# Performance work log

Hardware: AMD Instinct MI355X
Metric: run time of the kernel (lower is better)

Reference implementation:

```python
import jax, jax.numpy as jnp
from jax import lax
import numpy as np

S = 2048      # seq_len
E = 1024      # embedding_dim
H = 512       # hidden per direction (hidden_dim // 2)
V = 50000     # vocab
T = 16        # tagset_size
START, STOP = 0, 1
NEG = -10000.0


def setup_inputs() -> dict:
    key = jax.random.key(0)
    ks = jax.random.split(key, 20)
    bound = 1.0 / np.sqrt(H)

    def u(k, shape):
        return jax.random.uniform(k, shape, minval=-bound, maxval=bound, dtype=jnp.float32)

    sentence = jax.random.randint(ks[0], (S,), 0, V)
    emb = jax.random.normal(ks[1], (V, E), dtype=jnp.float32) * 0.1
    # PyTorch LSTM weights, gate order (i, f, g, o) stacked along first dim
    Wih_f = u(ks[2], (4 * H, E)); Whh_f = u(ks[3], (4 * H, H))
    bih_f = u(ks[4], (4 * H,));   bhh_f = u(ks[5], (4 * H,))
    Wih_b = u(ks[6], (4 * H, E)); Whh_b = u(ks[7], (4 * H, H))
    bih_b = u(ks[8], (4 * H,));   bhh_b = u(ks[9], (4 * H,))
    # init_hidden(): randn initial (h0, c0), [2 directions, H] (batch=1 squeezed)
    h0 = jax.random.normal(ks[10], (2, H), dtype=jnp.float32)
    c0 = jax.random.normal(ks[11], (2, H), dtype=jnp.float32)
    Wout = u(ks[12], (T, 2 * H)); bout = u(ks[13], (T,))
    transitions = jax.random.normal(ks[14], (T, T), dtype=jnp.float32)
    transitions = transitions.at[START, :].set(NEG).at[:, STOP].set(NEG)
    return dict(sentence=sentence, emb=emb,
                Wih_f=Wih_f, Whh_f=Whh_f, bih_f=bih_f, bhh_f=bhh_f,
                Wih_b=Wih_b, Whh_b=Whh_b, bih_b=bih_b, bhh_b=bhh_b,
                h0=h0, c0=c0, Wout=Wout, bout=bout, transitions=transitions)


def _lstm_dir(x, Wih, Whh, bih, bhh, h0, c0):
    # x: [S, E] -> hs: [S, H]; PyTorch gate order i, f, g, o
    xg = x @ Wih.T + bih + bhh  # precompute input contribution [S, 4H]

    def step(carry, xg_t):
        h, c = carry
        g = xg_t + h @ Whh.T
        i, f, gg, o = jnp.split(g, 4)
        i, f, o = jax.nn.sigmoid(i), jax.nn.sigmoid(f), jax.nn.sigmoid(o)
        c = f * c + i * jnp.tanh(gg)
        h = o * jnp.tanh(c)
        return (h, c), h

    _, hs = lax.scan(step, (h0, c0), xg)
    return hs


def _feats(sentence, emb, Wih_f, Whh_f, bih_f, bhh_f, Wih_b, Whh_b, bih_b, bhh_b,
           h0, c0, Wout, bout):
    x = emb[sentence]  # [S, E]
    hf = _lstm_dir(x, Wih_f, Whh_f, bih_f, bhh_f, h0[0], c0[0])              # [S, H]
    hb = _lstm_dir(x[::-1], Wih_b, Whh_b, bih_b, bhh_b, h0[1], c0[1])[::-1]  # [S, H]
    out = jnp.concatenate([hf, hb], axis=-1)  # [S, 2H]
    return out @ Wout.T + bout                # [S, T]


def _viterbi(feats, transitions):
    v0 = jnp.full((T,), NEG, dtype=feats.dtype).at[START].set(0.0)

    def vstep(v, feat):
        scores = v[None, :] + transitions        # [T(next), T(prev)]
        bp = jnp.argmax(scores, axis=1)          # best prev tag per next tag
        v_new = jnp.max(scores, axis=1) + feat
        return v_new, bp

    v, bps = lax.scan(vstep, v0, feats)          # bps: [S, T]
    terminal = v + transitions[STOP]
    best = jnp.argmax(terminal)
    path_score = terminal[best]

    def btstep(tag, bp):
        return bp[tag], tag

    _, path = lax.scan(btstep, best, bps, reverse=True)  # path[t] = tag at t
    return path_score, path


def reference(sentence, emb, Wih_f, Whh_f, bih_f, bhh_f, Wih_b, Whh_b, bih_b, bhh_b,
              h0, c0, Wout, bout, transitions):
    feats = _feats(sentence, emb, Wih_f, Whh_f, bih_f, bhh_f,
                   Wih_b, Whh_b, bih_b, bhh_b, h0, c0, Wout, bout)
    path_score, path = _viterbi(feats, transitions)
    return path_score, path
```

## Files before the change

### kernel.cpp

```cpp
#include <hip/hip_runtime.h>
#include <hip/hip_bf16.h>

#define S 2048
#define NEGV -10000.0f

typedef unsigned long long ull;
typedef unsigned int uint4v __attribute__((ext_vector_type(4)));

__device__ __forceinline__ float fsig(float x) {
  return 1.0f / (1.0f + __expf(-x));
}
__device__ __forceinline__ float ftanh(float x) {
  float a = fabsf(x);
  float e = __expf(-2.0f * a);
  float r = (1.0f - e) / (1.0f + e);
  return copysignf(r, x);
}

__global__ void clear_flags_k(int* __restrict__ flags) {
  flags[blockIdx.x * 256 + threadIdx.x] = 0;
}

__global__ void init_h_k(const float* __restrict__ h0, ull* __restrict__ hbuf) {
  int dir = blockIdx.x;
  int u = threadIdx.x;
  ull pk = (1ULL << 32) | (ull)__float_as_uint(h0[dir * 512 + u]);
  __hip_atomic_store(&hbuf[dir * 1024 + u], pk, __ATOMIC_RELAXED, __HIP_MEMORY_SCOPE_AGENT);
  __hip_atomic_store(&hbuf[dir * 1024 + 512 + u], 0ULL, __ATOMIC_RELAXED, __HIP_MEMORY_SCOPE_AGENT);
}

__global__ __launch_bounds__(256) void fused_k(
    const int* __restrict__ sent, const float* __restrict__ emb,
    const float* __restrict__ Wih_f, const float* __restrict__ Wih_b,
    const float* __restrict__ bih_f, const float* __restrict__ bhh_f,
    const float* __restrict__ bih_b, const float* __restrict__ bhh_b,
    const float* __restrict__ Whh_f, const float* __restrict__ Whh_b,
    const float* __restrict__ c0,
    float* __restrict__ xg,
    ull* __restrict__ hbuf,
    float* __restrict__ hs_cat,
    int* __restrict__ flags)
{
  __shared__ __align__(16) float smem[4544];
  const int t = threadIdx.x;

  if (blockIdx.x >= 128) {
    float* Asm = smem;
    float* Bsm = smem + 2304;
    int*   sidx = (int*)(smem + 4480);
    const int tm = t >> 4, tn = t & 15;
    const int lr = t >> 2, lkq = t & 3;

    for (int i = 0; i < 16; ++i) {
      const int T = (blockIdx.x - 128) + 128 * i;
      const int byo = T >> 6, bxo = T & 63;
      const int by = (byo & 1) ? (31 - (byo >> 1)) : (byo >> 1);
      const int bx = (bxo & 1) ? (32 + (bxo >> 1)) : (bxo >> 1);
      const int n0 = bx * 64, m0 = by * 64;

      const float* W = (n0 < 2048) ? (Wih_f + (size_t)n0 * 1024)
                                   : (Wih_b + (size_t)(n0 - 2048) * 1024);
      __syncthreads();
      if (t < 64) sidx[t] = sent[m0 + t];
      __syncthreads();

      float acc[4][4] = {};
      for (int k0 = 0; k0 < 1024; k0 += 32) {
        const float* ap = emb + (size_t)sidx[lr] * 1024 + k0 + lkq * 8;
        float4 a0 = *(const float4*)ap;
        float4 a1 = *(const float4*)(ap + 4);
        const float* bp = W + (size_t)lr * 1024 + k0 + lkq * 8;
        float4 b0 = *(const float4*)bp;
        float4 b1 = *(const float4*)(bp + 4);
        __syncthreads();
        *(float4*)&Asm[lr * 36 + lkq * 8]     = a0;
        *(float4*)&Asm[lr * 36 + lkq * 8 + 4] = a1;
        {
          const float* bb0 = (const float*)&b0;
          const float* bb1 = (const float*)&b1;
          #pragma unroll
          for (int j = 0; j < 4; ++j) Bsm[(lkq * 8 + j) * 68 + lr] = bb0[j];
          #pragma unroll
          for (int j = 0; j < 4; ++j) Bsm[(lkq * 8 + 4 + j) * 68 + lr] = bb1[j];
        }
        __syncthreads();
        #pragma unroll
        for (int kk = 0; kk < 32; ++kk) {
          float a0_ = Asm[(tm * 4 + 0) * 36 + kk];
          float a1_ = Asm[(tm * 4 + 1) * 36 + kk];
          float a2_ = Asm[(tm * 4 + 2) * 36 + kk];
          float a3_ = Asm[(tm * 4 + 3) * 36 + kk];
          float4 bv = *(const float4*)&Bsm[kk * 68 + tn * 4];
          acc[0][0] = fmaf(a0_, bv.x, acc[0][0]); acc[0][1] = fmaf(a0_, bv.y, acc[0][1]);
          acc[0][2] = fmaf(a0_, bv.z, acc[0][2]); acc[0][3] = fmaf(a0_, bv.w, acc[0][3]);
          acc[1][0] = fmaf(a1_, bv.x, acc[1][0]); acc[1][1] = fmaf(a1_, bv.y, acc[1][1]);
          acc[1][2] = fmaf(a1_, bv.z, acc[1][2]); acc[1][3] = fmaf(a1_, bv.w, acc[1][3]);
          acc[2][0] = fmaf(a2_, bv.x, acc[2][0]); acc[2][1] = fmaf(a2_, bv.y, acc[2][1]);
          acc[2][2] = fmaf(a2_, bv.z, acc[2][2]); acc[2][3] = fmaf(a2_, bv.w, acc[2][3]);
          acc[3][0] = fmaf(a3_, bv.x, acc[3][0]); acc[3][1] = fmaf(a3_, bv.y, acc[3][1]);
          acc[3][2] = fmaf(a3_, bv.z, acc[3][2]); acc[3][3] = fmaf(a3_, bv.w, acc[3][3]);
        }
      }

      const float* bi = (n0 < 2048) ? bih_f : bih_b;
      const float* bh = (n0 < 2048) ? bhh_f : bhh_b;
      const int nb = (n0 < 2048) ? n0 : (n0 - 2048);
      #pragma unroll
      for (int ii = 0; ii < 4; ++ii) {
        int m = m0 + tm * 4 + ii;
        #pragma unroll
        for (int j = 0; j < 4; ++j) {
          int nn = tn * 4 + j;
          float bias = bi[nb + nn] + bh[nb + nn];
          __hip_atomic_store(&xg[(size_t)m * 4096 + n0 + nn], acc[ii][j] + bias,
                             __ATOMIC_RELAXED, __HIP_MEMORY_SCOPE_AGENT);
        }
      }
      asm volatile("s_waitcnt vmcnt(0)" ::: "memory");
      __syncthreads();
      if (t == 0)
        __hip_atomic_store(&flags[by * 64 + bx], 1, __ATOMIC_RELAXED, __HIP_MEMORY_SCOPE_AGENT);
    }
    return;
  }

  const int w = blockIdx.x;
  const int dir = w & 1;
  const int wid = w >> 1;
  const int rr = t >> 3;
  const int seg = t & 7;
  const int g  = rr & 3;
  const int ul = rr >> 2;
  const int unit = wid * 8 + ul;
  const int grow = g * 512 + unit;
  const int bxf  = dir * 32 + g * 8 + (wid >> 3);

  float (*h_lds)[544] = (float(*)[544])smem;

  const float* Whh = dir ? Whh_b : Whh_f;
  float wreg[64];
  {
    const float* src = Whh + (size_t)grow * 512 + seg * 64;
    #pragma unroll
    for (int j = 0; j < 16; ++j) {
      float4 v = *(const float4*)(src + j * 4);
      wreg[4 * j + 0] = v.x; wreg[4 * j + 1] = v.y;
      wreg[4 * j + 2] = v.z; wreg[4 * j + 3] = v.w;
    }
  }

  ull* hb = hbuf + dir * 1024;
  float c_reg = c0[dir * 512 + unit];

  const int u0 = t * 2;
  const int wchunk = u0 >> 6, wpos = u0 & 63;

  float xg_a = 0.0f, xg_b = 0.0f;
  if (seg == 0) {
    int by0 = dir ? 31 : 0;
    while (__hip_atomic_load(&flags[by0 * 64 + bxf], __ATOMIC_RELAXED,
                             __HIP_MEMORY_SCOPE_AGENT) != 1)
      __builtin_amdgcn_s_sleep(8);
    int r0 = dir ? (S - 1) : 0;
    int r1 = dir ? (S - 2) : 1;
    xg_a = __hip_atomic_load(&xg[(size_t)r0 * 4096 + dir * 2048 + grow],
                             __ATOMIC_RELAXED, __HIP_MEMORY_SCOPE_AGENT);
    xg_b = __hip_atomic_load(&xg[(size_t)r1 * 4096 + dir * 2048 + grow],
                             __ATOMIC_RELAXED, __HIP_MEMORY_SCOPE_AGENT);
  }

  #define LSTM_STEP(K, XG_REG)                                                  \
  {                                                                             \
    const int k = (K);                                                          \
    float xgv = XG_REG;                                                         \
    if (seg == 0 && k + 2 < S) {            \
      int rowk = dir ? (S - 3 - k) : (k + 2);                                   \
      if ((rowk & 63) == (dir ? 63 : 0)) {       \
        int byn = rowk >> 6;                                                    \
        while (__hip_atomic_load(&flags[byn * 64 + bxf], __ATOMIC_RELAXED,      \
                                 __HIP_MEMORY_SCOPE_AGENT) != 1)                \
          __builtin_amdgcn_s_sleep(8);                                          \
      }                                                                         \
      XG_REG = __hip_atomic_load(&xg[(size_t)rowk * 4096 + dir * 2048 + grow],  \
                                 __ATOMIC_RELAXED, __HIP_MEMORY_SCOPE_AGENT);   \
    }                                                                           \
         \
    {                                                                           \
      ull* src = hb + (k & 1) * 512 + u0;                                       \
      const unsigned want = (unsigned)(k + 1);                                  \
      uint4v v;                                                                 \
      asm volatile("global_load_dwordx4 %0, %1, off sc0 sc1"                    \
                   : "=v"(v) : "v"(src) : "memory");                            \
      asm volatile("s_waitcnt vmcnt(0)" ::: "memory");                          \
      while (v.y != want || v.w != want) {                                      \
        __builtin_amdgcn_s_sleep(1);                                            \
        asm volatile("global_load_dwordx4 %0, %1, off sc0 sc1"                  \
                     : "=v"(v) : "v"(src) : "memory");                          \
        asm volatile("s_waitcnt vmcnt(0)" ::: "memory");                        \
      }                                                                         \
      float* dst = &h_lds[k & 1][wchunk * 68 + wpos];                           \
      dst[0] = __uint_as_float(v.x);                                            \
      dst[1] = __uint_as_float(v.z);                                            \
    }                                                                           \
    __syncthreads();                                                            \
                                         \
    const float* hl = &h_lds[k & 1][0];                                         \
    float p0 = 0.f, p1 = 0.f, p2 = 0.f, p3 = 0.f;                               \
    const float4* h4 = (const float4*)(hl + seg * 68);                          \
    _Pragma("unroll")                                                           \
    for (int j = 0; j < 16; ++j) {                                              \
      float4 hv = h4[j];                                                        \
      p0 = fmaf(wreg[4 * j + 0], hv.x, p0);                                     \
      p1 = fmaf(wreg[4 * j + 1], hv.y, p1);                                     \
      p2 = fmaf(wreg[4 * j + 2], hv.z, p2);                                     \
      p3 = fmaf(wreg[4 * j + 3], hv.w, p3);                                     \
    }                                                                           \
    float p = (p0 + p1) + (p2 + p3) + xgv;                                      \
    p += __shfl_xor(p, 1);                                                      \
    p += __shfl_xor(p, 2);                                                      \
    p += __shfl_xor(p, 4);                                                      \
    float gb_ = __shfl_xor(p, 8);                                 \
    float gc_ = __shfl_xor(p, 16);                                \
    float gd_ = __shfl_xor(gb_, 16);                              \
    if (g == 0) {                                                               \
      float iv = fsig(p), fv = fsig(gb_), ov = fsig(gd_);                       \
      float gv = ftanh(gc_);                                                    \
      c_reg = fv * c_reg + iv * gv;                                             \
      float hv = ov * ftanh(c_reg);                                             \
      if (seg == 0) {                                                           \
        ull pk = ((ull)(unsigned)(k + 2) << 32) | (ull)__float_as_uint(hv);     \
        __hip_atomic_store(&hb[((k + 1) & 1) * 512 + unit], pk,                 \
                           __ATOMIC_RELAXED, __HIP_MEMORY_SCOPE_AGENT);         \
        int orig = dir ? (S - 1 - k) : k;                                       \
        hs_cat[(size_t)orig * 1024 + dir * 512 + unit] = hv;                    \
      }                                                                         \
    }                                                                           \
  }

  for (int kk = 0; kk < S; kk += 2) {
    LSTM_STEP(kk, xg_a);
    LSTM_STEP(kk + 1, xg_b);
  }
  #undef LSTM_STEP
}

__global__ __launch_bounds__(64) void feats_k(
    const float* __restrict__ hs_cat, const float* __restrict__ Wout,
    const float* __restrict__ bout, float* __restrict__ feats)
{
  int tpos = blockIdx.x;
  int l = threadIdx.x;
  int j = l & 15, q = l >> 4;
  const float* h = hs_cat + (size_t)tpos * 1024 + q * 256;
  const float* wv = Wout + (size_t)j * 1024 + q * 256;
  float s = 0.f;
  #pragma unroll 8
  for (int i = 0; i < 256; i += 4) {
    float4 hv = *(const float4*)(h + i);
    float4 ww = *(const float4*)(wv + i);
    s = fmaf(hv.x, ww.x, s); s = fmaf(hv.y, ww.y, s);
    s = fmaf(hv.z, ww.z, s); s = fmaf(hv.w, ww.w, s);
  }
  s += __shfl_xor(s, 16);
  s += __shfl_xor(s, 32);
  if (q == 0) feats[tpos * 16 + j] = s + bout[j];
}

__global__ __launch_bounds__(64, 1) void viterbi_k(
    const float* __restrict__ feats, const float* __restrict__ trans,
    float* __restrict__ out)
{
  __shared__ __align__(16) float fch[2][256 * 16];
  __shared__ unsigned char bp4[S * 8];
  __shared__ float v_lds[2][16];

  const int l = threadIdx.x;
  const int next = l & 15, q = l >> 4;

  float tr0 = trans[next * 16 + q * 4 + 0];
  float tr1 = trans[next * 16 + q * 4 + 1];
  float tr2 = trans[next * 16 + q * 4 + 2];
  float tr3 = trans[next * 16 + q * 4 + 3];

  if (l < 16) v_lds[0][l] = (l == 0) ? 0.0f : NEGV;

  const float4* f4 = (const float4*)feats;
  float4 buf[16];
  #pragma unroll
  for (int i = 0; i < 16; ++i) buf[i] = f4[i * 64 + l];
  #pragma unroll
  for (int i = 0; i < 16; ++i) ((float4*)fch[0])[i * 64 + l] = buf[i];
  __syncthreads();

  for (int c = 0; c < 8; ++c) {
    if (c < 7) {
      #pragma unroll
      for (int i = 0; i < 16; ++i) buf[i] = f4[(c + 1) * 1024 + i * 64 + l];
    }
    const float* fc = fch[c & 1];
    for (int tt = 0; tt < 256; ++tt) {
      int t = c * 256 + tt;
      int pb = t & 1;
      const float* vin = v_lds[pb];
      float m = vin[q * 4 + 0] + tr0; int mi = q * 4;
      float s1 = vin[q * 4 + 1] + tr1; if (s1 > m) { m = s1; mi = q * 4 + 1; }
      float s2 = vin[q * 4 + 2] + tr2; if (s2 > m) { m = s2; mi = q * 4 + 2; }
      float s3 = vin[q * 4 + 3] + tr3; if (s3 > m) { m = s3; mi = q * 4 + 3; }
      #pragma unroll
      for (int mask = 16; mask <= 32; mask <<= 1) {
        float om = __shfl_xor(m, mask);
        int omi = __shfl_xor(mi, mask);
        if (om > m || (om == m && omi < mi)) { m = om; mi = omi; }
      }
      int pmi = __shfl_xor(mi, 1);
      if (q == 0) {
        v_lds[pb ^ 1][next] = m + fc[tt * 16 + next];
        if ((next & 1) == 0)
          bp4[t * 8 + (next >> 1)] = (unsigned char)((mi & 15) | ((pmi & 15) << 4));
      }
      __syncthreads();
    }
    if (c < 7) {
      #pragma unroll
      for (int i = 0; i < 16; ++i) ((float4*)fch[(c + 1) & 1])[i * 64 + l] = buf[i];
      __syncthreads();
    }
  }

  float term = (l < 16) ? (v_lds[0][l] + trans[1 * 16 + l]) : -3.0e38f;
  int ti = (l < 16) ? l : 0;
  #pragma unroll
  for (int mask = 1; mask <= 32; mask <<= 1) {
    float om = __shfl_xor(term, mask);
    int omi = __shfl_xor(ti, mask);
    if (om > term || (om == term && omi < ti)) { term = om; ti = omi; }
  }
  if (l == 0) {
    out[0] = term;
    int tag = ti;
    out[1 + (S - 1)] = (float)tag;
    for (int t = S - 1; t >= 1; --t) {
      tag = (bp4[t * 8 + (tag >> 1)] >> ((tag & 1) * 4)) & 15;
      out[t] = (float)tag;
    }
  }
}

extern "C" void kernel_launch(void* const* d_in, const int* in_sizes, int n_in,
                              void* d_out, int out_size, void* d_ws, size_t ws_size,
                              hipStream_t stream) {
  const int*   sent  = (const int*)d_in[0];
  const float* emb   = (const float*)d_in[1];
  const float* Wih_f = (const float*)d_in[2];
  const float* Whh_f = (const float*)d_in[3];
  const float* bih_f = (const float*)d_in[4];
  const float* bhh_f = (const float*)d_in[5];
  const float* Wih_b = (const float*)d_in[6];
  const float* Whh_b = (const float*)d_in[7];
  const float* bih_b = (const float*)d_in[8];
  const float* bhh_b = (const float*)d_in[9];
  const float* h0    = (const float*)d_in[10];
  const float* c0    = (const float*)d_in[11];
  const float* Wout  = (const float*)d_in[12];
  const float* bout  = (const float*)d_in[13];
  const float* trans = (const float*)d_in[14];
  float* out = (float*)d_out;

  char* ws = (char*)d_ws;
  float* xg     = (float*)(ws);
  float* hs_cat = (float*)(ws + 33554432);
  float* feats  = (float*)(ws + 41943040);
  ull*   hbuf   = (ull*)  (ws + 42074112);
  int*   flags  = (int*)  (ws + 42090496);

  clear_flags_k<<<8, 256, 0, stream>>>(flags);
  init_h_k<<<2, 512, 0, stream>>>(h0, hbuf);
  fused_k<<<256, 256, 0, stream>>>(sent, emb, Wih_f, Wih_b, bih_f, bhh_f,
                                   bih_b, bhh_b, Whh_f, Whh_b, c0,
                                   xg, hbuf, hs_cat, flags);
  feats_k<<<2048, 64, 0, stream>>>(hs_cat, Wout, bout, feats);
  viterbi_k<<<1, 64, 0, stream>>>(feats, trans, out);
}
```

Measured before the change: 3.921 ms.

## Replicate LSTM hidden-state broadcast buffer and pipeline polling loads

Each produced hidden value is now written to 8 replicated copies of the exchange buffer. Consumer blocks poll the replica chosen by their wave index, which spreads the polling traffic that all blocks previously aimed at one set of cache lines. The poll loop keeps two outstanding loads in flight instead of issuing one load and waiting on it. The two init kernels are merged into one launch, and the flags region is moved to make room for the replicas. In exchange, producers issue 8 atomic stores per step, adding write traffic to the critical recurrence path.

```diff
diff --git a/kernel.cpp b/kernel.cpp
--- a/kernel.cpp
+++ b/kernel.cpp
@@ -3,6 +3,8 @@
 
 #define S 2048
 #define NEGV -10000.0f
+#define REPS 8
+#define REPSTRIDE 2112
 
 typedef unsigned long long ull;
 typedef unsigned int uint4v __attribute__((ext_vector_type(4)));
@@ -17,16 +19,20 @@
   return copysignf(r, x);
 }
 
-__global__ void clear_flags_k(int* __restrict__ flags) {
-  flags[blockIdx.x * 256 + threadIdx.x] = 0;
-}
-
-__global__ void init_h_k(const float* __restrict__ h0, ull* __restrict__ hbuf) {
-  int dir = blockIdx.x;
-  int u = threadIdx.x;
-  ull pk = (1ULL << 32) | (ull)__float_as_uint(h0[dir * 512 + u]);
-  __hip_atomic_store(&hbuf[dir * 1024 + u], pk, __ATOMIC_RELAXED, __HIP_MEMORY_SCOPE_AGENT);
-  __hip_atomic_store(&hbuf[dir * 1024 + 512 + u], 0ULL, __ATOMIC_RELAXED, __HIP_MEMORY_SCOPE_AGENT);
+__global__ void init_k(const float* __restrict__ h0, ull* __restrict__ hbuf,
+                       int* __restrict__ flags) {
+  int b = blockIdx.x, u = threadIdx.x;
+  if (b < 16) {
+    int rep = b >> 1, dir = b & 1;
+    ull* base = hbuf + rep * REPSTRIDE + dir * 1024;
+    ull pk = (1ULL << 32) | (ull)__float_as_uint(h0[dir * 512 + u]);
+    __hip_atomic_store(&base[u], pk, __ATOMIC_RELAXED, __HIP_MEMORY_SCOPE_AGENT);
+    __hip_atomic_store(&base[512 + u], 0ULL, __ATOMIC_RELAXED, __HIP_MEMORY_SCOPE_AGENT);
+  } else {
+    int i = (b - 16) * 1024 + u;
+    flags[i] = 0;
+    flags[i + 512] = 0;
+  }
 }
 
 __global__ __launch_bounds__(256) void fused_k(
@@ -149,7 +155,9 @@
     }
   }
 
-  ull* hb = hbuf + dir * 1024;
+  ull* hbr = hbuf + (wid & 7) * REPSTRIDE + dir * 1024;
+  ull* hbp = hbuf + dir * 1024;
+
   float c_reg = c0[dir * 512 + unit];
 
   const int u0 = t * 2;
@@ -184,23 +192,36 @@
       XG_REG = __hip_atomic_load(&xg[(size_t)rowk * 4096 + dir * 2048 + grow],  \
                                  __ATOMIC_RELAXED, __HIP_MEMORY_SCOPE_AGENT);   \
     }                                                                           \
-         \
+        \
     {                                                                           \
-      ull* src = hb + (k & 1) * 512 + u0;                                       \
+      ull* src = hbr + (k & 1) * 512 + u0;                                      \
       const unsigned want = (unsigned)(k + 1);                                  \
-      uint4v v;                                                                 \
+      uint4v va, vb;                                                            \
+      asm volatile("s_waitcnt vmcnt(0)" ::: "memory");     \
       asm volatile("global_load_dwordx4 %0, %1, off sc0 sc1"                    \
-                   : "=v"(v) : "v"(src) : "memory");                            \
-      asm volatile("s_waitcnt vmcnt(0)" ::: "memory");                          \
-      while (v.y != want || v.w != want) {                                      \
-        __builtin_amdgcn_s_sleep(1);                                            \
+                   : "=v"(va) : "v"(src) : "memory");                           \
+      __builtin_amdgcn_s_sleep(4);                            \
+      asm volatile("global_load_dwordx4 %0, %1, off sc0 sc1"                    \
+                   : "=v"(vb) : "v"(src) : "memory");                           \
+      for (;;) {                                                                \
+        asm volatile("s_waitcnt vmcnt(1)" : "+v"(va) :: "memory");              \
+        if (va.y == want && va.w == want) {                                     \
+          asm volatile("s_waitcnt vmcnt(0)" : "+v"(va) :: "memory");            \
+          vb = va; break;                                                       \
+        }                                                                       \
         asm volatile("global_load_dwordx4 %0, %1, off sc0 sc1"                  \
-                     : "=v"(v) : "v"(src) : "memory");                          \
-        asm volatile("s_waitcnt vmcnt(0)" ::: "memory");                        \
+                     : "=v"(va) : "v"(src) : "memory");                         \
+        asm volatile("s_waitcnt vmcnt(1)" : "+v"(vb) :: "memory");              \
+        if (vb.y == want && vb.w == want) {                                     \
+          asm volatile("s_waitcnt vmcnt(0)" : "+v"(vb) :: "memory");            \
+          break;                                                                \
+        }                                                                       \
+        asm volatile("global_load_dwordx4 %0, %1, off sc0 sc1"                  \
+                     : "=v"(vb) : "v"(src) : "memory");                         \
       }                                                                         \
       float* dst = &h_lds[k & 1][wchunk * 68 + wpos];                           \
-      dst[0] = __uint_as_float(v.x);                                            \
-      dst[1] = __uint_as_float(v.z);                                            \
+      dst[0] = __uint_as_float(vb.x);                                           \
+      dst[1] = __uint_as_float(vb.z);                                           \
     }                                                                           \
     __syncthreads();                                                            \
                                          \
@@ -229,8 +250,11 @@
       float hv = ov * ftanh(c_reg);                                             \
       if (seg == 0) {                                                           \
         ull pk = ((ull)(unsigned)(k + 2) << 32) | (ull)__float_as_uint(hv);     \
-        __hip_atomic_store(&hb[((k + 1) & 1) * 512 + unit], pk,                 \
-                           __ATOMIC_RELAXED, __HIP_MEMORY_SCOPE_AGENT);         \
+        ull* pb = hbp + ((k + 1) & 1) * 512 + unit;                             \
+        _Pragma("unroll")                                                       \
+        for (int rp = 0; rp < REPS; ++rp)                                       \
+          __hip_atomic_store(pb + rp * REPSTRIDE, pk,                           \
+                             __ATOMIC_RELAXED, __HIP_MEMORY_SCOPE_AGENT);       \
         int orig = dir ? (S - 1 - k) : k;                                       \
         hs_cat[(size_t)orig * 1024 + dir * 512 + unit] = hv;                    \
       }                                                                         \
@@ -371,10 +395,9 @@
   float* hs_cat = (float*)(ws + 33554432);
   float* feats  = (float*)(ws + 41943040);
   ull*   hbuf   = (ull*)  (ws + 42074112);
-  int*   flags  = (int*)  (ws + 42090496);
-
-  clear_flags_k<<<8, 256, 0, stream>>>(flags);
-  init_h_k<<<2, 512, 0, stream>>>(h0, hbuf);
+  int*   flags  = (int*)  (ws + 42209280);
+
+  init_k<<<18, 512, 0, stream>>>(h0, hbuf, flags);
   fused_k<<<256, 256, 0, stream>>>(sent, emb, Wih_f, Wih_b, bih_f, bhh_f,
                                    bih_b, bhh_b, Whh_f, Whh_b, c0,
                                    xg, hbuf, hs_cat, flags);
```

Measured after the change: 4.513 ms. 15.1% more time.

## Parallelize Viterbi backtrace via map composition and keep forward pass in registers

Applied to the files above, without the earlier changes.

The Viterbi forward pass now keeps the score vector in registers and exchanges it with shuffles instead of LDS plus a block barrier per step. Backpointers are packed into one 64-bit map per timestep using ballots. The serial single-thread backtrace becomes a parallel one: each lane composes 32 maps, a shuffle prefix scan combines them, and each lane then writes its own segment. The two init kernels are merged into one launch. The cost is extra integer work for map composition and feats loads issued straight from global memory.

```diff
diff --git a/kernel.cpp b/kernel.cpp
--- a/kernel.cpp
+++ b/kernel.cpp
@@ -17,16 +17,16 @@
   return copysignf(r, x);
 }
 
-__global__ void clear_flags_k(int* __restrict__ flags) {
-  flags[blockIdx.x * 256 + threadIdx.x] = 0;
-}
-
-__global__ void init_h_k(const float* __restrict__ h0, ull* __restrict__ hbuf) {
-  int dir = blockIdx.x;
-  int u = threadIdx.x;
-  ull pk = (1ULL << 32) | (ull)__float_as_uint(h0[dir * 512 + u]);
-  __hip_atomic_store(&hbuf[dir * 1024 + u], pk, __ATOMIC_RELAXED, __HIP_MEMORY_SCOPE_AGENT);
-  __hip_atomic_store(&hbuf[dir * 1024 + 512 + u], 0ULL, __ATOMIC_RELAXED, __HIP_MEMORY_SCOPE_AGENT);
+__global__ void init_k(const float* __restrict__ h0, ull* __restrict__ hbuf,
+                       int* __restrict__ flags) {
+  int b = blockIdx.x, u = threadIdx.x;
+  if (b < 2) {
+    ull pk = (1ULL << 32) | (ull)__float_as_uint(h0[b * 512 + u]);
+    __hip_atomic_store(&hbuf[b * 1024 + u], pk, __ATOMIC_RELAXED, __HIP_MEMORY_SCOPE_AGENT);
+    __hip_atomic_store(&hbuf[b * 1024 + 512 + u], 0ULL, __ATOMIC_RELAXED, __HIP_MEMORY_SCOPE_AGENT);
+  } else {
+    flags[(b - 2) * 512 + u] = 0;
+  }
 }
 
 __global__ __launch_bounds__(256) void fused_k(
@@ -266,84 +266,113 @@
   if (q == 0) feats[tpos * 16 + j] = s + bout[j];
 }
 
+__device__ __forceinline__ ull compose_map(ull a, ull b) {
+  ull r = 0;
+  #pragma unroll
+  for (int i = 0; i < 16; ++i) {
+    int bi = (int)((b >> (4 * i)) & 15);
+    int ai = (int)((a >> (4 * bi)) & 15);
+    r |= (ull)ai << (4 * i);
+  }
+  return r;
+}
+
+__device__ __forceinline__ ull spread16(ull x) {
+  x &= 0xFFFFULL;
+  x = (x | (x << 24)) & 0x000000FF000000FFULL;
+  x = (x | (x << 12)) & 0x000F000F000F000FULL;
+  x = (x | (x << 6))  & 0x0303030303030303ULL;
+  x = (x | (x << 3))  & 0x1111111111111111ULL;
+  return x;
+}
+
 __global__ __launch_bounds__(64, 1) void viterbi_k(
     const float* __restrict__ feats, const float* __restrict__ trans,
     float* __restrict__ out)
 {
-  __shared__ __align__(16) float fch[2][256 * 16];
-  __shared__ unsigned char bp4[S * 8];
-  __shared__ float v_lds[2][16];
-
+  __shared__ ull bpm[S];
   const int l = threadIdx.x;
-  const int next = l & 15, q = l >> 4;
-
-  float tr0 = trans[next * 16 + q * 4 + 0];
-  float tr1 = trans[next * 16 + q * 4 + 1];
-  float tr2 = trans[next * 16 + q * 4 + 2];
-  float tr3 = trans[next * 16 + q * 4 + 3];
-
-  if (l < 16) v_lds[0][l] = (l == 0) ? 0.0f : NEGV;
-
-  const float4* f4 = (const float4*)feats;
-  float4 buf[16];
+  const int next = l & 15, q4 = (l >> 4) * 4;
+
+  const float tr0 = trans[next * 16 + q4 + 0];
+  const float tr1 = trans[next * 16 + q4 + 1];
+  const float tr2 = trans[next * 16 + q4 + 2];
+  const float tr3 = trans[next * 16 + q4 + 3];
+
+  float vcur = (next == 0) ? 0.0f : NEGV;
+
+  #define VSTEP(T, FREG)                                                        \
+  {                                                                             \
+    float pv0 = __shfl(vcur, q4 + 0, 16);                                       \
+    float pv1 = __shfl(vcur, q4 + 1, 16);                                       \
+    float pv2 = __shfl(vcur, q4 + 2, 16);                                       \
+    float pv3 = __shfl(vcur, q4 + 3, 16);                                       \
+    float m = pv0 + tr0; int mi = q4;                                           \
+    float s1 = pv1 + tr1; if (s1 > m) { m = s1; mi = q4 + 1; }                  \
+    float s2 = pv2 + tr2; if (s2 > m) { m = s2; mi = q4 + 2; }                  \
+    float s3 = pv3 + tr3; if (s3 > m) { m = s3; mi = q4 + 3; }                  \
+    { float om = __shfl_xor(m, 16); int omi = __shfl_xor(mi, 16);               \
+      if (om > m || (om == m && omi < mi)) { m = om; mi = omi; } }              \
+    { float om = __shfl_xor(m, 32); int omi = __shfl_xor(mi, 32);               \
+      if (om > m || (om == m && omi < mi)) { m = om; mi = omi; } }              \
+    vcur = m + (FREG);                                                          \
+    ull b0 = __ballot(mi & 1) & 0xFFFFULL;                                      \
+    ull b1 = __ballot(mi & 2) & 0xFFFFULL;                                      \
+    ull b2 = __ballot(mi & 4) & 0xFFFFULL;                                      \
+    ull b3 = __ballot(mi & 8) & 0xFFFFULL;                                      \
+    ull map = spread16(b0) | (spread16(b1) << 1) |                              \
+              (spread16(b2) << 2) | (spread16(b3) << 3);                        \
+    if (l == 0) bpm[T] = map;                                                   \
+  }
+
+  float f0 = feats[0 * 16 + next], f1 = feats[1 * 16 + next];
+  float f2 = feats[2 * 16 + next], f3 = feats[3 * 16 + next];
+  float f4 = feats[4 * 16 + next], f5 = feats[5 * 16 + next];
+  float f6 = feats[6 * 16 + next], f7 = feats[7 * 16 + next];
+
+  for (int t = 0; t < S; t += 8) {
+    VSTEP(t + 0, f0); if (t + 8  < S) f0 = feats[(t + 8)  * 16 + next];
+    VSTEP(t + 1, f1); if (t + 9  < S) f1 = feats[(t + 9)  * 16 + next];
+    VSTEP(t + 2, f2); if (t + 10 < S) f2 = feats[(t + 10) * 16 + next];
+    VSTEP(t + 3, f3); if (t + 11 < S) f3 = feats[(t + 11) * 16 + next];
+    VSTEP(t + 4, f4); if (t + 12 < S) f4 = feats[(t + 12) * 16 + next];
+    VSTEP(t + 5, f5); if (t + 13 < S) f5 = feats[(t + 13) * 16 + next];
+    VSTEP(t + 6, f6); if (t + 14 < S) f6 = feats[(t + 14) * 16 + next];
+    VSTEP(t + 7, f7); if (t + 15 < S) f7 = feats[(t + 15) * 16 + next];
+  }
+  #undef VSTEP
+
+  float term = vcur + trans[16 + next];
+  int ti = next;
   #pragma unroll
-  for (int i = 0; i < 16; ++i) buf[i] = f4[i * 64 + l];
-  #pragma unroll
-  for (int i = 0; i < 16; ++i) ((float4*)fch[0])[i * 64 + l] = buf[i];
-  __syncthreads();
-
-  for (int c = 0; c < 8; ++c) {
-    if (c < 7) {
-      #pragma unroll
-      for (int i = 0; i < 16; ++i) buf[i] = f4[(c + 1) * 1024 + i * 64 + l];
-    }
-    const float* fc = fch[c & 1];
-    for (int tt = 0; tt < 256; ++tt) {
-      int t = c * 256 + tt;
-      int pb = t & 1;
-      const float* vin = v_lds[pb];
-      float m = vin[q * 4 + 0] + tr0; int mi = q * 4;
-      float s1 = vin[q * 4 + 1] + tr1; if (s1 > m) { m = s1; mi = q * 4 + 1; }
-      float s2 = vin[q * 4 + 2] + tr2; if (s2 > m) { m = s2; mi = q * 4 + 2; }
-      float s3 = vin[q * 4 + 3] + tr3; if (s3 > m) { m = s3; mi = q * 4 + 3; }
-      #pragma unroll
-      for (int mask = 16; mask <= 32; mask <<= 1) {
-        float om = __shfl_xor(m, mask);
-        int omi = __shfl_xor(mi, mask);
-        if (om > m || (om == m && omi < mi)) { m = om; mi = omi; }
-      }
-      int pmi = __shfl_xor(mi, 1);
-      if (q == 0) {
-        v_lds[pb ^ 1][next] = m + fc[tt * 16 + next];
-        if ((next & 1) == 0)
-          bp4[t * 8 + (next >> 1)] = (unsigned char)((mi & 15) | ((pmi & 15) << 4));
-      }
-      __syncthreads();
-    }
-    if (c < 7) {
-      #pragma unroll
-      for (int i = 0; i < 16; ++i) ((float4*)fch[(c + 1) & 1])[i * 64 + l] = buf[i];
-      __syncthreads();
-    }
-  }
-
-  float term = (l < 16) ? (v_lds[0][l] + trans[1 * 16 + l]) : -3.0e38f;
-  int ti = (l < 16) ? l : 0;
-  #pragma unroll
-  for (int mask = 1; mask <= 32; mask <<= 1) {
+  for (int mask = 1; mask <= 8; mask <<= 1) {
     float om = __shfl_xor(term, mask);
     int omi = __shfl_xor(ti, mask);
     if (om > term || (om == term && omi < ti)) { term = om; ti = omi; }
   }
-  if (l == 0) {
-    out[0] = term;
-    int tag = ti;
-    out[1 + (S - 1)] = (float)tag;
-    for (int t = S - 1; t >= 1; --t) {
-      tag = (bp4[t * 8 + (tag >> 1)] >> ((tag & 1) * 4)) & 15;
-      out[t] = (float)tag;
-    }
-  }
+
+  __syncthreads();
+
+  ull M = bpm[32 * l + 31];
+  for (int i = 30; i >= 0; --i) M = compose_map(bpm[32 * l + i], M);
+
+  ull Sm = M;
+  #pragma unroll
+  for (int d = 1; d < 64; d <<= 1) {
+    ull o = __shfl_down(Sm, d);
+    if (l + d < 64) Sm = compose_map(Sm, o);
+  }
+  ull G = __shfl_down(Sm, 1);
+  if (l == 63) G = 0xFEDCBA9876543210ULL;
+
+  int cur = (int)((G >> (4 * ti)) & 15);
+  for (int i = 31; i >= 1; --i) {
+    int t = 32 * l + i;
+    out[1 + t] = (float)cur;
+    cur = (int)((bpm[t] >> (4 * cur)) & 15);
+  }
+  out[1 + 32 * l] = (float)cur;
+  if (l == 0) out[0] = term;
 }
 
 extern "C" void kernel_launch(void* const* d_in, const int* in_sizes, int n_in,
@@ -373,8 +402,7 @@
   ull*   hbuf   = (ull*)  (ws + 42074112);
   int*   flags  = (int*)  (ws + 42090496);
 
-  clear_flags_k<<<8, 256, 0, stream>>>(flags);
-  init_h_k<<<2, 512, 0, stream>>>(h0, hbuf);
+  init_k<<<6, 512, 0, stream>>>(h0, hbuf, flags);
   fused_k<<<256, 256, 0, stream>>>(sent, emb, Wih_f, Wih_b, bih_f, bhh_f,
                                    bih_b, bhh_b, Whh_f, Whh_b, c0,
                                    xg, hbuf, hs_cat, flags);
```

Measured after the change: 3.919 ms. Within noise of the previous version (-0.1%).
